# Optimization experiments

Measured on AMD Instinct MI355X. Metric: run time of the kernel, lower is better.

Reference implementation:

```python
import jax, jax.numpy as jnp
import numpy as np

WINDOW = 2  # hardcoded global in the original module


def band_count(seq_len, window=WINDOW):
    """C[a,b] = number of positions i whose local window covers both a and b.
    Windows (from converse_qk): i=0 -> [0, W]; i=1 -> [0, W+1];
    i=seq-2 -> [seq-W-2, seq-1]; i=seq-1 -> [seq-W-1, seq-1]; else [i-W, i+W].
    """
    i = jnp.arange(seq_len)
    lo = jnp.clip(i - window, 0, None)
    hi = jnp.clip(i + window, None, seq_len - 1)
    lo = jnp.where(i == 1, 0, lo)
    hi = jnp.where(i == 1, window + 1, hi)
    lo = jnp.where(i == seq_len - 2, seq_len - window - 2, lo)
    hi = jnp.where(i == seq_len - 2, seq_len - 1, hi)
    a = jnp.arange(seq_len)[None, :]
    M = ((a >= lo[:, None]) & (a <= hi[:, None])).astype(jnp.float32)  # [i, a]
    return M.T @ M  # [seq, seq]


def setup_inputs() -> dict:
    key = jax.random.key(0)
    ks = jax.random.split(key, 12)
    bs, seq, d_model = 2, 2048, 512
    s = 1.0 / np.sqrt(d_model)
    inp = {
        'q': jax.random.normal(ks[0], (bs, seq, d_model), jnp.float32),
        'k': jax.random.normal(ks[1], (bs, seq, d_model), jnp.float32),
        'v': jax.random.normal(ks[2], (bs, seq, d_model), jnp.float32),
        'Wq': jax.random.normal(ks[3], (d_model, d_model), jnp.float32) * s,
        'bq': jnp.zeros((d_model,), jnp.float32),
        'Wk': jax.random.normal(ks[4], (d_model, d_model), jnp.float32) * s,
        'bk': jnp.zeros((d_model,), jnp.float32),
        'Wv': jax.random.normal(ks[5], (d_model, d_model), jnp.float32) * s,
        'bv': jnp.zeros((d_model,), jnp.float32),
        'Wo': jax.random.normal(ks[6], (d_model, d_model), jnp.float32) * s,
        'bo': jnp.zeros((d_model,), jnp.float32),
    }
    return inp


def reference(q, k, v, Wq, bq, Wk, bk, Wv, bv, Wo, bo):
    bs, seq, d_model = q.shape
    heads = 8
    d_k = d_model // heads
    # projections (torch Linear uses x @ W.T + b; here W stored already transposed)
    qh = (q @ Wq + bq).reshape(bs, seq, heads, d_k).transpose(0, 2, 1, 3)
    kh = (k @ Wk + bk).reshape(bs, seq, heads, d_k).transpose(0, 2, 1, 3)
    vh = (v @ Wv + bv).reshape(bs, seq, heads, d_k).transpose(0, 2, 1, 3)
    C = band_count(seq)  # [seq, seq] window-overlap counts
    scores = jnp.einsum('bhqd,bhkd->bhqk', qh, kh) / jnp.sqrt(jnp.float32(d_k))
    scores = scores * C  # banded count-weighted scores; zeros outside band
    attn = jax.nn.softmax(scores, axis=-1)  # full-row softmax, as in original
    out = jnp.einsum('bhqk,bhkd->bhqd', attn, vh)
    concat = out.transpose(0, 2, 1, 3).reshape(bs, seq, d_model)
    return concat @ Wo + bo
```

## Files before the change

### kernel.cpp

```cpp
#include <hip/hip_runtime.h>
#include <hip/hip_bf16.h>

#define SEQ 2048
#define DM  512
#define BS  2
#define NH  8
#define DK  64
#define MROWS (BS * SEQ)
#define GK 64

typedef __attribute__((ext_vector_type(8))) short bf16x8;
typedef __attribute__((ext_vector_type(4))) float f32x4;

__device__ __forceinline__ unsigned short f2bf(float f) {
    unsigned int u = __float_as_uint(f);
    u += 0x7fff + ((u >> 16) & 1);
    return (unsigned short)(u >> 16);
}
__device__ __forceinline__ float bf2f(unsigned short b) {
    return __uint_as_float((unsigned int)b << 16);
}

#define GLDS16(g, l) __builtin_amdgcn_global_load_lds( \
    (const __attribute__((address_space(1))) void*)(g), \
    (__attribute__((address_space(3))) void*)(unsigned int)(unsigned long long)(l), 16, 0, 0)

__global__ __launch_bounds__(256) void prep_w(const float* __restrict__ Wq, const float* __restrict__ Wk,
                                              const float* __restrict__ Wv, const float* __restrict__ Wo,
                                              const float* __restrict__ bv_,
                                              unsigned short* __restrict__ WqT, unsigned short* __restrict__ WkT,
                                              unsigned short* __restrict__ WvT, unsigned short* __restrict__ WoT,
                                              float* __restrict__ vsum)
{
    __shared__ float tile[32][33];
    const int bid = blockIdx.x;
    if (bid == 0) {
        #pragma unroll
        for (int t = 0; t < 4; ++t) {
            const int idx = threadIdx.x * 4 + t;
            vsum[idx] = (float)SEQ * bv_[idx & (DM - 1)];
        }
    }
    const int z = bid >> 8;
    const int tl = bid & 255;
    const float* W = (z == 0) ? Wq : (z == 1) ? Wk : (z == 2) ? Wv : Wo;
    unsigned short* T = (z == 0) ? WqT : (z == 1) ? WkT : (z == 2) ? WvT : WoT;
    const int n0 = (tl & 15) * 32, k0 = (tl >> 4) * 32;
    const int tx = threadIdx.x & 31;
    const int ty = threadIdx.x >> 5;
    #pragma unroll
    for (int r = 0; r < 32; r += 8)
        tile[ty + r][tx] = W[(size_t)(k0 + ty + r) * DM + n0 + tx];
    __syncthreads();
    #pragma unroll
    for (int r = 0; r < 32; r += 8)
        T[(size_t)(n0 + ty + r) * DM + k0 + tx] = f2bf(tile[tx][ty + r]);
}

__global__ __launch_bounds__(256) void gemm_qkv_cvt(const float* __restrict__ q,
                                                    const float* __restrict__ k,
                                                    const float* __restrict__ v,
                                                    const unsigned short* __restrict__ WqT,
                                                    const unsigned short* __restrict__ WkT,
                                                    const unsigned short* __restrict__ WvT,
                                                    const float* __restrict__ bq, const float* __restrict__ bk,
                                                    const float* __restrict__ bvp,
                                                    unsigned short* __restrict__ Qb, unsigned short* __restrict__ Kb,
                                                    unsigned short* __restrict__ Vb, float* __restrict__ vsum)
{
    __shared__ unsigned short S[12288];

    const int g = blockIdx.x;
    const int xcd   = g & 7;
    const int n_idx = (g >> 3) & 3;
    const int t     = g >> 5;
    const int strip = t * 8 + xcd;
    const int z     = strip >> 6;
    const int m0    = (strip & 63) * 64;
    const int n0    = n_idx * 128;

    const float* Af; const unsigned short* BT; const float* bias; unsigned short* C; float* vs;
    if (z == 0)      { Af = q; BT = WqT; bias = bq; C = Qb; vs = nullptr; }
    else if (z == 1) { Af = k; BT = WkT; bias = bk; C = Kb; vs = nullptr; }
    else             { Af = v; BT = WvT; bias = bvp; C = Vb; vs = vsum; }

    const int tid  = threadIdx.x;
    const int lane = tid & 63;
    const int wave = tid >> 6;
    const int wm = (wave & 1) * 32;
    const int wn = (wave >> 1) * 64;
    const int l15 = lane & 15;
    const int q8  = (lane >> 4) * 8;

    f32x4 acc[2][4];
    #pragma unroll
    for (int i = 0; i < 2; ++i)
        #pragma unroll
        for (int j = 0; j < 4; ++j)
            acc[i][j] = (f32x4){0.f, 0.f, 0.f, 0.f};

    const int arow = tid >> 4;
    const int akl  = (tid & 15) * 4;
    const int awoff = ((akl >> 5) * 2048) + (akl & 31);

    const unsigned short* gb[4];
    unsigned short* lb[4];
    #pragma unroll
    for (int it = 0; it < 4; ++it) {
        const int c = tid + it * 256;
        const int n  = (c >> 2) & 127;
        const int kk = c >> 9;
        gb[it] = BT + (size_t)(n0 + n) * DM + kk * 32 + (c & 3) * 8;
        lb[it] = &S[4096 + c * 8];
    }

    for (int k0 = 0; k0 < DM; k0 += GK) {
        #pragma unroll
        for (int it = 0; it < 4; ++it)
            GLDS16(gb[it] + k0, lb[it]);

        float4 av[4];
        #pragma unroll
        for (int p = 0; p < 4; ++p)
            av[p] = *(const float4*)(Af + (size_t)(m0 + p * 16 + arow) * DM + k0 + akl);
        #pragma unroll
        for (int p = 0; p < 4; ++p) {
            ushort4 o;
            o.x = f2bf(av[p].x); o.y = f2bf(av[p].y); o.z = f2bf(av[p].z); o.w = f2bf(av[p].w);
            *(ushort4*)&S[awoff + (p * 16 + arow) * 32] = o;
        }
        __syncthreads();

        #pragma unroll
        for (int kk = 0; kk < 2; ++kk) {
            bf16x8 af[2], bfr[4];
            #pragma unroll
            for (int i = 0; i < 2; ++i)
                af[i] = *(const bf16x8*)&S[kk * 2048 + (wm + i * 16 + l15) * 32 + q8];
            #pragma unroll
            for (int j = 0; j < 4; ++j)
                bfr[j] = *(const bf16x8*)&S[4096 + kk * 4096 + (wn + j * 16 + l15) * 32 + q8];
            #pragma unroll
            for (int i = 0; i < 2; ++i)
                #pragma unroll
                for (int j = 0; j < 4; ++j)
                    acc[i][j] = __builtin_amdgcn_mfma_f32_16x16x32_bf16(af[i], bfr[j], acc[i][j], 0, 0, 0);
        }
        __syncthreads();
    }

    #pragma unroll
    for (int j = 0; j < 4; ++j) {
        const int col = n0 + wn + j * 16 + l15;
        const float bv = bias[col];
        #pragma unroll
        for (int i = 0; i < 2; ++i) {
            const int rbase = m0 + wm + i * 16 + (lane >> 4) * 4;
            #pragma unroll
            for (int r = 0; r < 4; ++r)
                C[(size_t)(rbase + r) * DM + col] = f2bf(acc[i][j][r] + bv);
        }
    }

    if (vs) {
        const int b = m0 >> 11;
        #pragma unroll
        for (int j = 0; j < 4; ++j) {
            float part = 0.f;
            #pragma unroll
            for (int i = 0; i < 2; ++i)
                #pragma unroll
                for (int r = 0; r < 4; ++r)
                    part += acc[i][j][r];
            part += __shfl_xor(part, 16, 64);
            part += __shfl_xor(part, 32, 64);
            if ((lane >> 4) == 0)
                atomicAdd(&vs[b * DM + n0 + wn + j * 16 + l15], part);
        }
    }
}

template<int TGM, int TGN, int WMT, int WNT>
__device__ __forceinline__ void gemm_core(const unsigned short* __restrict__ A,
                                          const unsigned short* __restrict__ BT,
                                          const float* __restrict__ bias,
                                          float* __restrict__ C,
                                          const int m0, const int n0)
{
    __shared__ unsigned short S[(TGM + TGN) * GK];

    const int tid  = threadIdx.x;
    const int lane = tid & 63;
    const int wave = tid >> 6;
    constexpr int WAVES_M = TGM / (WMT * 16);
    const int wm = (wave % WAVES_M) * (WMT * 16);
    const int wn = (wave / WAVES_M) * (WNT * 16);
    const int l15 = lane & 15;
    const int q8  = (lane >> 4) * 8;

    f32x4 acc[WMT][WNT];
    #pragma unroll
    for (int i = 0; i < WMT; ++i)
        #pragma unroll
        for (int j = 0; j < WNT; ++j)
            acc[i][j] = (f32x4){0.f, 0.f, 0.f, 0.f};

    constexpr int NCH = (TGM + TGN) * 8;
    constexpr int NIT = NCH / 256;
    const unsigned short* gp[NIT];
    unsigned short* lp[NIT];
    #pragma unroll
    for (int it = 0; it < NIT; ++it) {
        const int c = tid + it * 256;
        if (c < TGM * 8) {
            const int kk = c / (TGM * 4);
            const int cr = c - kk * (TGM * 4);
            gp[it] = A + (size_t)(m0 + (cr >> 2)) * DM + kk * 32 + (cr & 3) * 8;
        } else {
            const int cb = c - TGM * 8;
            const int kk = cb / (TGN * 4);
            const int cr = cb - kk * (TGN * 4);
            gp[it] = BT + (size_t)(n0 + (cr >> 2)) * DM + kk * 32 + (cr & 3) * 8;
        }
        lp[it] = &S[(size_t)c * 8];
    }

    for (int k0 = 0; k0 < DM; k0 += GK) {
        #pragma unroll
        for (int it = 0; it < NIT; ++it)
            GLDS16(gp[it] + k0, lp[it]);
        __syncthreads();

        #pragma unroll
        for (int kk = 0; kk < 2; ++kk) {
            bf16x8 af[WMT], bfr[WNT];
            #pragma unroll
            for (int i = 0; i < WMT; ++i)
                af[i] = *(const bf16x8*)&S[kk * TGM * 32 + (wm + i * 16 + l15) * 32 + q8];
            #pragma unroll
            for (int j = 0; j < WNT; ++j)
                bfr[j] = *(const bf16x8*)&S[TGM * 64 + kk * TGN * 32 + (wn + j * 16 + l15) * 32 + q8];
            #pragma unroll
            for (int i = 0; i < WMT; ++i)
                #pragma unroll
                for (int j = 0; j < WNT; ++j)
                    acc[i][j] = __builtin_amdgcn_mfma_f32_16x16x32_bf16(af[i], bfr[j], acc[i][j], 0, 0, 0);
        }
        __syncthreads();
    }

    #pragma unroll
    for (int j = 0; j < WNT; ++j) {
        const int col = n0 + wn + j * 16 + l15;
        const float bv = bias[col];
        #pragma unroll
        for (int i = 0; i < WMT; ++i) {
            const int rbase = m0 + wm + i * 16 + (lane >> 4) * 4;
            #pragma unroll
            for (int r = 0; r < 4; ++r)
                C[(size_t)(rbase + r) * DM + col] = acc[i][j][r] + bv;
        }
    }
}

__global__ __launch_bounds__(256) void gemm_out(const unsigned short* A, const unsigned short* BT,
                                                const float* bias, float* C)
{
    const int g = blockIdx.x;
    const int xcd   = g & 7;
    const int n_idx = (g >> 3) & 7;
    const int m_idx = (g >> 6) * 8 + xcd;
    gemm_core<64, 64, 2, 2>(A, BT, bias, C, m_idx * 64, n_idx * 64);
}

__global__ __launch_bounds__(64) void attn_mfma(const unsigned short* __restrict__ Qb,
                                                const unsigned short* __restrict__ Kb,
                                                const unsigned short* __restrict__ Vb,
                                                const float* __restrict__ vsum,
                                                unsigned short* __restrict__ concat)
{
    __shared__ unsigned short Wlds[16 * 32];
    const int lane = threadIdx.x;
    const int l15  = lane & 15;
    const int quad = lane >> 4;
    const int bh = blockIdx.y;
    const int b = bh >> 3, h = bh & 7;
    const int q0 = blockIdx.x * 16;
    const size_t rowbase = (size_t)b * SEQ;
    const int dbase = h * DK;

    const unsigned short* qrow = Qb + (rowbase + q0 + l15) * DM + dbase + quad * 8;
    const bf16x8 aq0 = *(const bf16x8*)(qrow);
    const bf16x8 aq1 = *(const bf16x8*)(qrow + 32);

    f32x4 sc[2];
    #pragma unroll
    for (int t = 0; t < 2; ++t) {
        int kp = q0 - 4 + t * 16 + l15;
        kp = min(max(kp, 0), SEQ - 1);
        const unsigned short* krow = Kb + (rowbase + kp) * DM + dbase + quad * 8;
        const bf16x8 b0 = *(const bf16x8*)(krow);
        const bf16x8 b1 = *(const bf16x8*)(krow + 32);
        f32x4 z = (f32x4){0.f, 0.f, 0.f, 0.f};
        z = __builtin_amdgcn_mfma_f32_16x16x32_bf16(aq0, b0, z, 0, 0, 0);
        sc[t] = __builtin_amdgcn_mfma_f32_16x16x32_bf16(aq1, b1, z, 0, 0, 0);
    }

    float dsum[4] = {0.f, 0.f, 0.f, 0.f};
    #pragma unroll
    for (int t = 0; t < 2; ++t) {
        const int kpos = q0 - 4 + t * 16 + l15;
        #pragma unroll
        for (int r = 0; r < 4; ++r) {
            const int qq = q0 + quad * 4 + r;
            const int mn = min(qq, kpos), mx = qq + kpos - mn;
            const float cnt = (float)(min(mn + 2, SEQ - 1) - max(mx - 2, 0) + 1);
            const float cw = (kpos >= 0 && kpos < SEQ && (mx - mn) <= 4) ? cnt * 0.125f : 0.f;
            const float w = expf(sc[t][r] * cw) - 1.f;
            const unsigned short wb = f2bf(w);
            Wlds[(quad * 4 + r) * 32 + t * 16 + l15] = wb;
            dsum[r] += bf2f(wb);
        }
    }
    #pragma unroll
    for (int off = 1; off <= 8; off <<= 1)
        #pragma unroll
        for (int r = 0; r < 4; ++r)
            dsum[r] += __shfl_xor(dsum[r], off, 64);

    __syncthreads();
    const bf16x8 aw = *(const bf16x8*)&Wlds[l15 * 32 + quad * 8];

    #pragma unroll
    for (int nt = 0; nt < 4; ++nt) {
        const int d = dbase + nt * 16 + l15;
        bf16x8 bv_;
        #pragma unroll
        for (int j = 0; j < 8; ++j) {
            int kr = q0 - 4 + quad * 8 + j;
            kr = min(max(kr, 0), SEQ - 1);
            bv_[j] = (short)Vb[(rowbase + kr) * DM + d];
        }
        f32x4 z = (f32x4){0.f, 0.f, 0.f, 0.f};
        const f32x4 o = __builtin_amdgcn_mfma_f32_16x16x32_bf16(aw, bv_, z, 0, 0, 0);
        const float vs = vsum[b * DM + d];
        #pragma unroll
        for (int r = 0; r < 4; ++r) {
            const float den = (float)SEQ + dsum[r];
            concat[(rowbase + q0 + quad * 4 + r) * DM + d] = f2bf((vs + o[r]) / den);
        }
    }
}

extern "C" void kernel_launch(void* const* d_in, const int* in_sizes, int n_in,
                              void* d_out, int out_size, void* d_ws, size_t ws_size,
                              hipStream_t stream) {
    const float* q  = (const float*)d_in[0];
    const float* k  = (const float*)d_in[1];
    const float* v  = (const float*)d_in[2];
    const float* Wq = (const float*)d_in[3];
    const float* bq = (const float*)d_in[4];
    const float* Wk = (const float*)d_in[5];
    const float* bk = (const float*)d_in[6];
    const float* Wv = (const float*)d_in[7];
    const float* bv = (const float*)d_in[8];
    const float* Wo = (const float*)d_in[9];
    const float* bo = (const float*)d_in[10];

    const size_t NE = (size_t)MROWS * DM;

    float* vsum = (float*)d_ws;
    unsigned short* Qb     = (unsigned short*)(vsum + 1024);
    unsigned short* Kb     = Qb + NE;
    unsigned short* Vb     = Kb + NE;
    unsigned short* WqT    = Vb + NE;
    unsigned short* WkT    = WqT + DM * DM;
    unsigned short* WvT    = WkT + DM * DM;
    unsigned short* WoT    = WvT + DM * DM;
    unsigned short* concat = WoT + DM * DM;

    prep_w<<<1024, 256, 0, stream>>>(Wq, Wk, Wv, Wo, bv, WqT, WkT, WvT, WoT, vsum);

    gemm_qkv_cvt<<<768, 256, 0, stream>>>(q, k, v, WqT, WkT, WvT,
                                          bq, bk, bv, Qb, Kb, Vb, vsum);

    attn_mfma<<<dim3(SEQ / 16, BS * NH), 64, 0, stream>>>(Qb, Kb, Vb, vsum, concat);

    gemm_out<<<512, 256, 0, stream>>>(concat, WoT, bo, (float*)d_out);
}
```

Baseline: 115.4 us.

## Fuse banded attention with output projection in one kernel

Combines the attention kernel and the output-projection GEMM. Each 512-thread block handles 16 query rows for all 8 heads, one wave per head, and writes the concat tile into shared memory. It then multiplies that tile by Wo directly, with each wave computing 64 output columns. This removes the concat round trip through global memory and one kernel launch. In exchange the grid shrinks to 256 blocks, and Wo is re-read from global or L2 by every block with no LDS staging.

```diff
diff --git a/kernel.cpp b/kernel.cpp
--- a/kernel.cpp
+++ b/kernel.cpp
@@ -180,114 +180,32 @@
     }
 }
 
-template<int TGM, int TGN, int WMT, int WNT>
-__device__ __forceinline__ void gemm_core(const unsigned short* __restrict__ A,
-                                          const unsigned short* __restrict__ BT,
-                                          const float* __restrict__ bias,
-                                          float* __restrict__ C,
-                                          const int m0, const int n0)
-{
-    __shared__ unsigned short S[(TGM + TGN) * GK];
-
-    const int tid  = threadIdx.x;
-    const int lane = tid & 63;
-    const int wave = tid >> 6;
-    constexpr int WAVES_M = TGM / (WMT * 16);
-    const int wm = (wave % WAVES_M) * (WMT * 16);
-    const int wn = (wave / WAVES_M) * (WNT * 16);
-    const int l15 = lane & 15;
-    const int q8  = (lane >> 4) * 8;
-
-    f32x4 acc[WMT][WNT];
-    #pragma unroll
-    for (int i = 0; i < WMT; ++i)
-        #pragma unroll
-        for (int j = 0; j < WNT; ++j)
-            acc[i][j] = (f32x4){0.f, 0.f, 0.f, 0.f};
-
-    constexpr int NCH = (TGM + TGN) * 8;
-    constexpr int NIT = NCH / 256;
-    const unsigned short* gp[NIT];
-    unsigned short* lp[NIT];
-    #pragma unroll
-    for (int it = 0; it < NIT; ++it) {
-        const int c = tid + it * 256;
-        if (c < TGM * 8) {
-            const int kk = c / (TGM * 4);
-            const int cr = c - kk * (TGM * 4);
-            gp[it] = A + (size_t)(m0 + (cr >> 2)) * DM + kk * 32 + (cr & 3) * 8;
-        } else {
-            const int cb = c - TGM * 8;
-            const int kk = cb / (TGN * 4);
-            const int cr = cb - kk * (TGN * 4);
-            gp[it] = BT + (size_t)(n0 + (cr >> 2)) * DM + kk * 32 + (cr & 3) * 8;
-        }
-        lp[it] = &S[(size_t)c * 8];
-    }
-
-    for (int k0 = 0; k0 < DM; k0 += GK) {
-        #pragma unroll
-        for (int it = 0; it < NIT; ++it)
-            GLDS16(gp[it] + k0, lp[it]);
-        __syncthreads();
-
-        #pragma unroll
-        for (int kk = 0; kk < 2; ++kk) {
-            bf16x8 af[WMT], bfr[WNT];
-            #pragma unroll
-            for (int i = 0; i < WMT; ++i)
-                af[i] = *(const bf16x8*)&S[kk * TGM * 32 + (wm + i * 16 + l15) * 32 + q8];
-            #pragma unroll
-            for (int j = 0; j < WNT; ++j)
-                bfr[j] = *(const bf16x8*)&S[TGM * 64 + kk * TGN * 32 + (wn + j * 16 + l15) * 32 + q8];
-            #pragma unroll
-            for (int i = 0; i < WMT; ++i)
-                #pragma unroll
-                for (int j = 0; j < WNT; ++j)
-                    acc[i][j] = __builtin_amdgcn_mfma_f32_16x16x32_bf16(af[i], bfr[j], acc[i][j], 0, 0, 0);
-        }
-        __syncthreads();
-    }
-
-    #pragma unroll
-    for (int j = 0; j < WNT; ++j) {
-        const int col = n0 + wn + j * 16 + l15;
-        const float bv = bias[col];
-        #pragma unroll
-        for (int i = 0; i < WMT; ++i) {
-            const int rbase = m0 + wm + i * 16 + (lane >> 4) * 4;
-            #pragma unroll
-            for (int r = 0; r < 4; ++r)
-                C[(size_t)(rbase + r) * DM + col] = acc[i][j][r] + bv;
-        }
-    }
-}
-
-__global__ __launch_bounds__(256) void gemm_out(const unsigned short* A, const unsigned short* BT,
-                                                const float* bias, float* C)
-{
-    const int g = blockIdx.x;
-    const int xcd   = g & 7;
-    const int n_idx = (g >> 3) & 7;
-    const int m_idx = (g >> 6) * 8 + xcd;
-    gemm_core<64, 64, 2, 2>(A, BT, bias, C, m_idx * 64, n_idx * 64);
-}
-
-__global__ __launch_bounds__(64) void attn_mfma(const unsigned short* __restrict__ Qb,
+__global__ __launch_bounds__(512) void attn_out(const unsigned short* __restrict__ Qb,
                                                 const unsigned short* __restrict__ Kb,
                                                 const unsigned short* __restrict__ Vb,
                                                 const float* __restrict__ vsum,
-                                                unsigned short* __restrict__ concat)
+                                                const unsigned short* __restrict__ WoT,
+                                                const float* __restrict__ bo,
+                                                float* __restrict__ out)
 {
-    __shared__ unsigned short Wlds[16 * 32];
-    const int lane = threadIdx.x;
+    __shared__ unsigned short Wc[16][520];
+    __shared__ unsigned short Wl[NH][16 * 32];
+
+    const int tid  = threadIdx.x;
+    const int lane = tid & 63;
+    const int h    = tid >> 6;
     const int l15  = lane & 15;
     const int quad = lane >> 4;
-    const int bh = blockIdx.y;
-    const int b = bh >> 3, h = bh & 7;
-    const int q0 = blockIdx.x * 16;
+    const int b  = blockIdx.x >> 7;
+    const int q0 = (blockIdx.x & 127) * 16;
     const size_t rowbase = (size_t)b * SEQ;
     const int dbase = h * DK;
+
+    const unsigned short* Bp = WoT + (size_t)(h * 64 + l15) * DM + quad * 8;
+    bf16x8 bpre[4];
+    #pragma unroll
+    for (int j = 0; j < 4; ++j)
+        bpre[j] = *(const bf16x8*)(Bp + (size_t)j * 16 * DM);
 
     const unsigned short* qrow = Qb + (rowbase + q0 + l15) * DM + dbase + quad * 8;
     const bf16x8 aq0 = *(const bf16x8*)(qrow);
@@ -318,7 +236,7 @@
             const float cw = (kpos >= 0 && kpos < SEQ && (mx - mn) <= 4) ? cnt * 0.125f : 0.f;
             const float w = expf(sc[t][r] * cw) - 1.f;
             const unsigned short wb = f2bf(w);
-            Wlds[(quad * 4 + r) * 32 + t * 16 + l15] = wb;
+            Wl[h][(quad * 4 + r) * 32 + t * 16 + l15] = wb;
             dsum[r] += bf2f(wb);
         }
     }
@@ -329,7 +247,7 @@
             dsum[r] += __shfl_xor(dsum[r], off, 64);
 
     __syncthreads();
-    const bf16x8 aw = *(const bf16x8*)&Wlds[l15 * 32 + quad * 8];
+    const bf16x8 aw = *(const bf16x8*)&Wl[h][l15 * 32 + quad * 8];
 
     #pragma unroll
     for (int nt = 0; nt < 4; ++nt) {
@@ -347,8 +265,35 @@
         #pragma unroll
         for (int r = 0; r < 4; ++r) {
             const float den = (float)SEQ + dsum[r];
-            concat[(rowbase + q0 + quad * 4 + r) * DM + d] = f2bf((vs + o[r]) / den);
-        }
+            Wc[quad * 4 + r][d] = f2bf((vs + o[r]) / den);
+        }
+    }
+
+    __syncthreads();
+
+    f32x4 acc[4];
+    #pragma unroll
+    for (int j = 0; j < 4; ++j)
+        acc[j] = (f32x4){0.f, 0.f, 0.f, 0.f};
+
+    #pragma unroll
+    for (int ks = 0; ks < 16; ++ks) {
+        const bf16x8 af = *(const bf16x8*)&Wc[l15][ks * 32 + quad * 8];
+        #pragma unroll
+        for (int j = 0; j < 4; ++j) {
+            const bf16x8 bw = (ks == 0) ? bpre[j]
+                            : *(const bf16x8*)(Bp + (size_t)j * 16 * DM + ks * 32);
+            acc[j] = __builtin_amdgcn_mfma_f32_16x16x32_bf16(af, bw, acc[j], 0, 0, 0);
+        }
+    }
+
+    #pragma unroll
+    for (int j = 0; j < 4; ++j) {
+        const int col = h * 64 + j * 16 + l15;
+        const float bov = bo[col];
+        #pragma unroll
+        for (int r = 0; r < 4; ++r)
+            out[(rowbase + q0 + quad * 4 + r) * DM + col] = acc[j][r] + bov;
     }
 }
 
@@ -377,14 +322,11 @@
     unsigned short* WkT    = WqT + DM * DM;
     unsigned short* WvT    = WkT + DM * DM;
     unsigned short* WoT    = WvT + DM * DM;
-    unsigned short* concat = WoT + DM * DM;
 
     prep_w<<<1024, 256, 0, stream>>>(Wq, Wk, Wv, Wo, bv, WqT, WkT, WvT, WoT, vsum);
 
     gemm_qkv_cvt<<<768, 256, 0, stream>>>(q, k, v, WqT, WkT, WvT,
                                           bq, bk, bv, Qb, Kb, Vb, vsum);
 
-    attn_mfma<<<dim3(SEQ / 16, BS * NH), 64, 0, stream>>>(Qb, Kb, Vb, vsum, concat);
-
-    gemm_out<<<512, 256, 0, stream>>>(concat, WoT, bo, (float*)d_out);
-}
+    attn_out<<<256, 512, 0, stream>>>(Qb, Kb, Vb, vsum, WoT, bo, (float*)d_out);
+}
```

After: 123.5 us. 7.1% more time.

## Fuse four kernels into two persistent kernels with software grid barriers

Applied to the files above, without the earlier changes.

Merges the weight transpose/convert with the QKV projection GEMM, and the banded attention with the output GEMM. Each pair runs in one launch, separated by an atomic-counter grid barrier, and a memset resets the counters. The goal is to remove two kernel launches and their inter-kernel gaps. It also switches the fp32-to-bf16 conversion of activations to packed v_cvt_pk_bf16_f32 instructions. The grid barrier relies on all 768 or 512 blocks being co-resident; if they are not, it deadlocks. The extra memset launch and the barrier spin add overhead.

```diff
diff --git a/kernel.cpp b/kernel.cpp
--- a/kernel.cpp
+++ b/kernel.cpp
@@ -25,50 +25,61 @@
     (const __attribute__((address_space(1))) void*)(g), \
     (__attribute__((address_space(3))) void*)(unsigned int)(unsigned long long)(l), 16, 0, 0)
 
-__global__ __launch_bounds__(256) void prep_w(const float* __restrict__ Wq, const float* __restrict__ Wk,
-                                              const float* __restrict__ Wv, const float* __restrict__ Wo,
-                                              const float* __restrict__ bv_,
-                                              unsigned short* __restrict__ WqT, unsigned short* __restrict__ WkT,
-                                              unsigned short* __restrict__ WvT, unsigned short* __restrict__ WoT,
-                                              float* __restrict__ vsum)
+__device__ __forceinline__ void gridbar(unsigned int* ctr, unsigned int target) {
+    __syncthreads();
+    if (threadIdx.x == 0) {
+        __hip_atomic_fetch_add(ctr, 1u, __ATOMIC_RELEASE, __HIP_MEMORY_SCOPE_AGENT);
+        while (__hip_atomic_load(ctr, __ATOMIC_RELAXED, __HIP_MEMORY_SCOPE_AGENT) < target)
+            __builtin_amdgcn_s_sleep(2);
+        (void)__hip_atomic_load(ctr, __ATOMIC_ACQUIRE, __HIP_MEMORY_SCOPE_AGENT);
+    }
+    __syncthreads();
+}
+
+__global__ __launch_bounds__(256, 3) void prep_qkv(
+    const float* __restrict__ q, const float* __restrict__ k, const float* __restrict__ v,
+    const float* __restrict__ Wq, const float* __restrict__ Wk,
+    const float* __restrict__ Wv, const float* __restrict__ Wo,
+    const float* __restrict__ bq, const float* __restrict__ bk, const float* __restrict__ bv_,
+    unsigned short* __restrict__ WqT, unsigned short* __restrict__ WkT,
+    unsigned short* __restrict__ WvT, unsigned short* __restrict__ WoT,
+    unsigned short* __restrict__ Qb, unsigned short* __restrict__ Kb,
+    unsigned short* __restrict__ Vb,
+    float* __restrict__ vsum, unsigned int* __restrict__ ctr)
 {
-    __shared__ float tile[32][33];
-    const int bid = blockIdx.x;
-    if (bid == 0) {
-        #pragma unroll
-        for (int t = 0; t < 4; ++t) {
-            const int idx = threadIdx.x * 4 + t;
-            vsum[idx] = (float)SEQ * bv_[idx & (DM - 1)];
-        }
-    }
-    const int z = bid >> 8;
-    const int tl = bid & 255;
-    const float* W = (z == 0) ? Wq : (z == 1) ? Wk : (z == 2) ? Wv : Wo;
-    unsigned short* T = (z == 0) ? WqT : (z == 1) ? WkT : (z == 2) ? WvT : WoT;
-    const int n0 = (tl & 15) * 32, k0 = (tl >> 4) * 32;
-    const int tx = threadIdx.x & 31;
-    const int ty = threadIdx.x >> 5;
-    #pragma unroll
-    for (int r = 0; r < 32; r += 8)
-        tile[ty + r][tx] = W[(size_t)(k0 + ty + r) * DM + n0 + tx];
-    __syncthreads();
-    #pragma unroll
-    for (int r = 0; r < 32; r += 8)
-        T[(size_t)(n0 + ty + r) * DM + k0 + tx] = f2bf(tile[tx][ty + r]);
-}
-
-__global__ __launch_bounds__(256) void gemm_qkv_cvt(const float* __restrict__ q,
-                                                    const float* __restrict__ k,
-                                                    const float* __restrict__ v,
-                                                    const unsigned short* __restrict__ WqT,
-                                                    const unsigned short* __restrict__ WkT,
-                                                    const unsigned short* __restrict__ WvT,
-                                                    const float* __restrict__ bq, const float* __restrict__ bk,
-                                                    const float* __restrict__ bvp,
-                                                    unsigned short* __restrict__ Qb, unsigned short* __restrict__ Kb,
-                                                    unsigned short* __restrict__ Vb, float* __restrict__ vsum)
-{
-    __shared__ unsigned short S[12288];
+    __shared__ __align__(16) unsigned char SMEM[24576];
+
+    {
+        float (*tile)[33] = (float (*)[33])SMEM;
+        if (blockIdx.x == 0) {
+            #pragma unroll
+            for (int t = 0; t < 4; ++t) {
+                const int idx = threadIdx.x * 4 + t;
+                vsum[idx] = (float)SEQ * bv_[idx & (DM - 1)];
+            }
+        }
+        const int tx = threadIdx.x & 31;
+        const int ty = threadIdx.x >> 5;
+        for (int tt = blockIdx.x; tt < 1024; tt += 768) {
+            const int z = tt >> 8;
+            const int tl = tt & 255;
+            const float* W = (z == 0) ? Wq : (z == 1) ? Wk : (z == 2) ? Wv : Wo;
+            unsigned short* T = (z == 0) ? WqT : (z == 1) ? WkT : (z == 2) ? WvT : WoT;
+            const int n0 = (tl & 15) * 32, k0 = (tl >> 4) * 32;
+            #pragma unroll
+            for (int r = 0; r < 32; r += 8)
+                tile[ty + r][tx] = W[(size_t)(k0 + ty + r) * DM + n0 + tx];
+            __syncthreads();
+            #pragma unroll
+            for (int r = 0; r < 32; r += 8)
+                T[(size_t)(n0 + ty + r) * DM + k0 + tx] = f2bf(tile[tx][ty + r]);
+            __syncthreads();
+        }
+    }
+
+    gridbar(ctr, 768);
+
+    unsigned short* S = (unsigned short*)SMEM;
 
     const int g = blockIdx.x;
     const int xcd   = g & 7;
@@ -82,7 +93,7 @@
     const float* Af; const unsigned short* BT; const float* bias; unsigned short* C; float* vs;
     if (z == 0)      { Af = q; BT = WqT; bias = bq; C = Qb; vs = nullptr; }
     else if (z == 1) { Af = k; BT = WkT; bias = bk; C = Kb; vs = nullptr; }
-    else             { Af = v; BT = WvT; bias = bvp; C = Vb; vs = vsum; }
+    else             { Af = v; BT = WvT; bias = bv_; C = Vb; vs = vsum; }
 
     const int tid  = threadIdx.x;
     const int lane = tid & 63;
@@ -125,9 +136,11 @@
             av[p] = *(const float4*)(Af + (size_t)(m0 + p * 16 + arow) * DM + k0 + akl);
         #pragma unroll
         for (int p = 0; p < 4; ++p) {
-            ushort4 o;
-            o.x = f2bf(av[p].x); o.y = f2bf(av[p].y); o.z = f2bf(av[p].z); o.w = f2bf(av[p].w);
-            *(ushort4*)&S[awoff + (p * 16 + arow) * 32] = o;
+            unsigned int u0, u1;
+            asm("v_cvt_pk_bf16_f32 %0, %1, %2" : "=v"(u0) : "v"(av[p].x), "v"(av[p].y));
+            asm("v_cvt_pk_bf16_f32 %0, %1, %2" : "=v"(u1) : "v"(av[p].z), "v"(av[p].w));
+            uint2 o; o.x = u0; o.y = u1;
+            *(uint2*)&S[awoff + (p * 16 + arow) * 32] = o;
         }
         __syncthreads();
 
@@ -152,13 +165,13 @@
     #pragma unroll
     for (int j = 0; j < 4; ++j) {
         const int col = n0 + wn + j * 16 + l15;
-        const float bv = bias[col];
+        const float bvv = bias[col];
         #pragma unroll
         for (int i = 0; i < 2; ++i) {
             const int rbase = m0 + wm + i * 16 + (lane >> 4) * 4;
             #pragma unroll
             for (int r = 0; r < 4; ++r)
-                C[(size_t)(rbase + r) * DM + col] = f2bf(acc[i][j][r] + bv);
+                C[(size_t)(rbase + r) * DM + col] = f2bf(acc[i][j][r] + bvv);
         }
     }
 
@@ -180,174 +193,168 @@
     }
 }
 
-template<int TGM, int TGN, int WMT, int WNT>
-__device__ __forceinline__ void gemm_core(const unsigned short* __restrict__ A,
-                                          const unsigned short* __restrict__ BT,
-                                          const float* __restrict__ bias,
-                                          float* __restrict__ C,
-                                          const int m0, const int n0)
+__global__ __launch_bounds__(256, 2) void attn_out2(
+    const unsigned short* __restrict__ Qb, const unsigned short* __restrict__ Kb,
+    const unsigned short* __restrict__ Vb, const float* __restrict__ vsum,
+    const unsigned short* __restrict__ WoT, const float* __restrict__ bo,
+    unsigned short* __restrict__ concat, float* __restrict__ out,
+    unsigned int* __restrict__ ctr)
 {
-    __shared__ unsigned short S[(TGM + TGN) * GK];
-
-    const int tid  = threadIdx.x;
-    const int lane = tid & 63;
-    const int wave = tid >> 6;
-    constexpr int WAVES_M = TGM / (WMT * 16);
-    const int wm = (wave % WAVES_M) * (WMT * 16);
-    const int wn = (wave / WAVES_M) * (WNT * 16);
-    const int l15 = lane & 15;
-    const int q8  = (lane >> 4) * 8;
-
-    f32x4 acc[WMT][WNT];
-    #pragma unroll
-    for (int i = 0; i < WMT; ++i)
-        #pragma unroll
-        for (int j = 0; j < WNT; ++j)
-            acc[i][j] = (f32x4){0.f, 0.f, 0.f, 0.f};
-
-    constexpr int NCH = (TGM + TGN) * 8;
-    constexpr int NIT = NCH / 256;
-    const unsigned short* gp[NIT];
-    unsigned short* lp[NIT];
-    #pragma unroll
-    for (int it = 0; it < NIT; ++it) {
-        const int c = tid + it * 256;
-        if (c < TGM * 8) {
-            const int kk = c / (TGM * 4);
-            const int cr = c - kk * (TGM * 4);
-            gp[it] = A + (size_t)(m0 + (cr >> 2)) * DM + kk * 32 + (cr & 3) * 8;
-        } else {
-            const int cb = c - TGM * 8;
-            const int kk = cb / (TGN * 4);
-            const int cr = cb - kk * (TGN * 4);
-            gp[it] = BT + (size_t)(n0 + (cr >> 2)) * DM + kk * 32 + (cr & 3) * 8;
-        }
-        lp[it] = &S[(size_t)c * 8];
-    }
-
-    for (int k0 = 0; k0 < DM; k0 += GK) {
-        #pragma unroll
-        for (int it = 0; it < NIT; ++it)
-            GLDS16(gp[it] + k0, lp[it]);
+    __shared__ __align__(16) unsigned char SMEM[16384];
+
+    {
+        unsigned short* Wlds = (unsigned short*)SMEM + (threadIdx.x >> 6) * 512;
+        const int lane = threadIdx.x & 63;
+        const int l15  = lane & 15;
+        const int quad = lane >> 4;
+        const int u  = blockIdx.x * 4 + (threadIdx.x >> 6);
+        const int bh = u >> 7;
+        const int b = bh >> 3, h = bh & 7;
+        const int q0 = (u & 127) * 16;
+        const size_t rowbase = (size_t)b * SEQ;
+        const int dbase = h * DK;
+
+        const unsigned short* qrow = Qb + (rowbase + q0 + l15) * DM + dbase + quad * 8;
+        const bf16x8 aq0 = *(const bf16x8*)(qrow);
+        const bf16x8 aq1 = *(const bf16x8*)(qrow + 32);
+
+        f32x4 sc[2];
+        #pragma unroll
+        for (int t = 0; t < 2; ++t) {
+            int kp = q0 - 4 + t * 16 + l15;
+            kp = min(max(kp, 0), SEQ - 1);
+            const unsigned short* krow = Kb + (rowbase + kp) * DM + dbase + quad * 8;
+            const bf16x8 b0 = *(const bf16x8*)(krow);
+            const bf16x8 b1 = *(const bf16x8*)(krow + 32);
+            f32x4 z = (f32x4){0.f, 0.f, 0.f, 0.f};
+            z = __builtin_amdgcn_mfma_f32_16x16x32_bf16(aq0, b0, z, 0, 0, 0);
+            sc[t] = __builtin_amdgcn_mfma_f32_16x16x32_bf16(aq1, b1, z, 0, 0, 0);
+        }
+
+        float dsum[4] = {0.f, 0.f, 0.f, 0.f};
+        #pragma unroll
+        for (int t = 0; t < 2; ++t) {
+            const int kpos = q0 - 4 + t * 16 + l15;
+            #pragma unroll
+            for (int r = 0; r < 4; ++r) {
+                const int qq = q0 + quad * 4 + r;
+                const int mn = min(qq, kpos), mx = qq + kpos - mn;
+                const float cnt = (float)(min(mn + 2, SEQ - 1) - max(mx - 2, 0) + 1);
+                const float cw = (kpos >= 0 && kpos < SEQ && (mx - mn) <= 4) ? cnt * 0.125f : 0.f;
+                const float w = expf(sc[t][r] * cw) - 1.f;
+                const unsigned short wb = f2bf(w);
+                Wlds[(quad * 4 + r) * 32 + t * 16 + l15] = wb;
+                dsum[r] += bf2f(wb);
+            }
+        }
+        #pragma unroll
+        for (int off = 1; off <= 8; off <<= 1)
+            #pragma unroll
+            for (int r = 0; r < 4; ++r)
+                dsum[r] += __shfl_xor(dsum[r], off, 64);
+
         __syncthreads();
-
-        #pragma unroll
-        for (int kk = 0; kk < 2; ++kk) {
-            bf16x8 af[WMT], bfr[WNT];
-            #pragma unroll
-            for (int i = 0; i < WMT; ++i)
-                af[i] = *(const bf16x8*)&S[kk * TGM * 32 + (wm + i * 16 + l15) * 32 + q8];
-            #pragma unroll
-            for (int j = 0; j < WNT; ++j)
-                bfr[j] = *(const bf16x8*)&S[TGM * 64 + kk * TGN * 32 + (wn + j * 16 + l15) * 32 + q8];
-            #pragma unroll
-            for (int i = 0; i < WMT; ++i)
-                #pragma unroll
-                for (int j = 0; j < WNT; ++j)
-                    acc[i][j] = __builtin_amdgcn_mfma_f32_16x16x32_bf16(af[i], bfr[j], acc[i][j], 0, 0, 0);
-        }
-        __syncthreads();
-    }
-
-    #pragma unroll
-    for (int j = 0; j < WNT; ++j) {
-        const int col = n0 + wn + j * 16 + l15;
-        const float bv = bias[col];
-        #pragma unroll
-        for (int i = 0; i < WMT; ++i) {
-            const int rbase = m0 + wm + i * 16 + (lane >> 4) * 4;
-            #pragma unroll
-            for (int r = 0; r < 4; ++r)
-                C[(size_t)(rbase + r) * DM + col] = acc[i][j][r] + bv;
-        }
-    }
-}
-
-__global__ __launch_bounds__(256) void gemm_out(const unsigned short* A, const unsigned short* BT,
-                                                const float* bias, float* C)
-{
-    const int g = blockIdx.x;
-    const int xcd   = g & 7;
-    const int n_idx = (g >> 3) & 7;
-    const int m_idx = (g >> 6) * 8 + xcd;
-    gemm_core<64, 64, 2, 2>(A, BT, bias, C, m_idx * 64, n_idx * 64);
-}
-
-__global__ __launch_bounds__(64) void attn_mfma(const unsigned short* __restrict__ Qb,
-                                                const unsigned short* __restrict__ Kb,
-                                                const unsigned short* __restrict__ Vb,
-                                                const float* __restrict__ vsum,
-                                                unsigned short* __restrict__ concat)
-{
-    __shared__ unsigned short Wlds[16 * 32];
-    const int lane = threadIdx.x;
-    const int l15  = lane & 15;
-    const int quad = lane >> 4;
-    const int bh = blockIdx.y;
-    const int b = bh >> 3, h = bh & 7;
-    const int q0 = blockIdx.x * 16;
-    const size_t rowbase = (size_t)b * SEQ;
-    const int dbase = h * DK;
-
-    const unsigned short* qrow = Qb + (rowbase + q0 + l15) * DM + dbase + quad * 8;
-    const bf16x8 aq0 = *(const bf16x8*)(qrow);
-    const bf16x8 aq1 = *(const bf16x8*)(qrow + 32);
-
-    f32x4 sc[2];
-    #pragma unroll
-    for (int t = 0; t < 2; ++t) {
-        int kp = q0 - 4 + t * 16 + l15;
-        kp = min(max(kp, 0), SEQ - 1);
-        const unsigned short* krow = Kb + (rowbase + kp) * DM + dbase + quad * 8;
-        const bf16x8 b0 = *(const bf16x8*)(krow);
-        const bf16x8 b1 = *(const bf16x8*)(krow + 32);
-        f32x4 z = (f32x4){0.f, 0.f, 0.f, 0.f};
-        z = __builtin_amdgcn_mfma_f32_16x16x32_bf16(aq0, b0, z, 0, 0, 0);
-        sc[t] = __builtin_amdgcn_mfma_f32_16x16x32_bf16(aq1, b1, z, 0, 0, 0);
-    }
-
-    float dsum[4] = {0.f, 0.f, 0.f, 0.f};
-    #pragma unroll
-    for (int t = 0; t < 2; ++t) {
-        const int kpos = q0 - 4 + t * 16 + l15;
-        #pragma unroll
-        for (int r = 0; r < 4; ++r) {
-            const int qq = q0 + quad * 4 + r;
-            const int mn = min(qq, kpos), mx = qq + kpos - mn;
-            const float cnt = (float)(min(mn + 2, SEQ - 1) - max(mx - 2, 0) + 1);
-            const float cw = (kpos >= 0 && kpos < SEQ && (mx - mn) <= 4) ? cnt * 0.125f : 0.f;
-            const float w = expf(sc[t][r] * cw) - 1.f;
-            const unsigned short wb = f2bf(w);
-            Wlds[(quad * 4 + r) * 32 + t * 16 + l15] = wb;
-            dsum[r] += bf2f(wb);
-        }
-    }
-    #pragma unroll
-    for (int off = 1; off <= 8; off <<= 1)
-        #pragma unroll
-        for (int r = 0; r < 4; ++r)
-            dsum[r] += __shfl_xor(dsum[r], off, 64);
-
-    __syncthreads();
-    const bf16x8 aw = *(const bf16x8*)&Wlds[l15 * 32 + quad * 8];
-
-    #pragma unroll
-    for (int nt = 0; nt < 4; ++nt) {
-        const int d = dbase + nt * 16 + l15;
-        bf16x8 bv_;
-        #pragma unroll
-        for (int j = 0; j < 8; ++j) {
-            int kr = q0 - 4 + quad * 8 + j;
-            kr = min(max(kr, 0), SEQ - 1);
-            bv_[j] = (short)Vb[(rowbase + kr) * DM + d];
-        }
-        f32x4 z = (f32x4){0.f, 0.f, 0.f, 0.f};
-        const f32x4 o = __builtin_amdgcn_mfma_f32_16x16x32_bf16(aw, bv_, z, 0, 0, 0);
-        const float vs = vsum[b * DM + d];
-        #pragma unroll
-        for (int r = 0; r < 4; ++r) {
-            const float den = (float)SEQ + dsum[r];
-            concat[(rowbase + q0 + quad * 4 + r) * DM + d] = f2bf((vs + o[r]) / den);
+        const bf16x8 aw = *(const bf16x8*)&Wlds[l15 * 32 + quad * 8];
+
+        #pragma unroll
+        for (int nt = 0; nt < 4; ++nt) {
+            const int d = dbase + nt * 16 + l15;
+            bf16x8 bv_;
+            #pragma unroll
+            for (int j = 0; j < 8; ++j) {
+                int kr = q0 - 4 + quad * 8 + j;
+                kr = min(max(kr, 0), SEQ - 1);
+                bv_[j] = (short)Vb[(rowbase + kr) * DM + d];
+            }
+            f32x4 z = (f32x4){0.f, 0.f, 0.f, 0.f};
+            const f32x4 o = __builtin_amdgcn_mfma_f32_16x16x32_bf16(aw, bv_, z, 0, 0, 0);
+            const float vsv = vsum[b * DM + d];
+            #pragma unroll
+            for (int r = 0; r < 4; ++r) {
+                const float den = (float)SEQ + dsum[r];
+                concat[(rowbase + q0 + quad * 4 + r) * DM + d] = f2bf((vsv + o[r]) / den);
+            }
+        }
+    }
+
+    gridbar(ctr, 512);
+
+    {
+        unsigned short* S = (unsigned short*)SMEM;
+        const int g = blockIdx.x;
+        const int xcd   = g & 7;
+        const int n_idx = (g >> 3) & 7;
+        const int m_idx = (g >> 6) * 8 + xcd;
+        const int m0 = m_idx * 64, n0 = n_idx * 64;
+
+        const int tid  = threadIdx.x;
+        const int lane = tid & 63;
+        const int wave = tid >> 6;
+        const int wm = (wave & 1) * 32;
+        const int wn = (wave >> 1) * 32;
+        const int l15 = lane & 15;
+        const int q8  = (lane >> 4) * 8;
+
+        f32x4 acc[2][2];
+        #pragma unroll
+        for (int i = 0; i < 2; ++i)
+            #pragma unroll
+            for (int j = 0; j < 2; ++j)
+                acc[i][j] = (f32x4){0.f, 0.f, 0.f, 0.f};
+
+        const unsigned short* gp[4];
+        unsigned short* lp[4];
+        #pragma unroll
+        for (int it = 0; it < 4; ++it) {
+            const int c = tid + it * 256;
+            if (c < 512) {
+                const int kk = c >> 8;
+                const int cr = c & 255;
+                gp[it] = concat + (size_t)(m0 + (cr >> 2)) * DM + kk * 32 + (c & 3) * 8;
+            } else {
+                const int cb = c - 512;
+                const int kk = cb >> 8;
+                const int cr = cb & 255;
+                gp[it] = WoT + (size_t)(n0 + (cr >> 2)) * DM + kk * 32 + (cb & 3) * 8;
+            }
+            lp[it] = &S[(size_t)c * 8];
+        }
+
+        for (int k0 = 0; k0 < DM; k0 += GK) {
+            #pragma unroll
+            for (int it = 0; it < 4; ++it)
+                GLDS16(gp[it] + k0, lp[it]);
+            __syncthreads();
+
+            #pragma unroll
+            for (int kk = 0; kk < 2; ++kk) {
+                bf16x8 af[2], bfr[2];
+                #pragma unroll
+                for (int i = 0; i < 2; ++i)
+                    af[i] = *(const bf16x8*)&S[kk * 2048 + (wm + i * 16 + l15) * 32 + q8];
+                #pragma unroll
+                for (int j = 0; j < 2; ++j)
+                    bfr[j] = *(const bf16x8*)&S[4096 + kk * 2048 + (wn + j * 16 + l15) * 32 + q8];
+                #pragma unroll
+                for (int i = 0; i < 2; ++i)
+                    #pragma unroll
+                    for (int j = 0; j < 2; ++j)
+                        acc[i][j] = __builtin_amdgcn_mfma_f32_16x16x32_bf16(af[i], bfr[j], acc[i][j], 0, 0, 0);
+            }
+            __syncthreads();
+        }
+
+        #pragma unroll
+        for (int j = 0; j < 2; ++j) {
+            const int col = n0 + wn + j * 16 + l15;
+            const float bov = bo[col];
+            #pragma unroll
+            for (int i = 0; i < 2; ++i) {
+                const int rbase = m0 + wm + i * 16 + (lane >> 4) * 4;
+                #pragma unroll
+                for (int r = 0; r < 4; ++r)
+                    out[(size_t)(rbase + r) * DM + col] = acc[i][j][r] + bov;
+            }
         }
     }
 }
@@ -369,7 +376,8 @@
 
     const size_t NE = (size_t)MROWS * DM;
 
-    float* vsum = (float*)d_ws;
+    unsigned int* ctrs = (unsigned int*)d_ws;
+    float* vsum = (float*)d_ws + 16;
     unsigned short* Qb     = (unsigned short*)(vsum + 1024);
     unsigned short* Kb     = Qb + NE;
     unsigned short* Vb     = Kb + NE;
@@ -379,12 +387,11 @@
     unsigned short* WoT    = WvT + DM * DM;
     unsigned short* concat = WoT + DM * DM;
 
-    prep_w<<<1024, 256, 0, stream>>>(Wq, Wk, Wv, Wo, bv, WqT, WkT, WvT, WoT, vsum);
-
-    gemm_qkv_cvt<<<768, 256, 0, stream>>>(q, k, v, WqT, WkT, WvT,
-                                          bq, bk, bv, Qb, Kb, Vb, vsum);
-
-    attn_mfma<<<dim3(SEQ / 16, BS * NH), 64, 0, stream>>>(Qb, Kb, Vb, vsum, concat);
-
-    gemm_out<<<512, 256, 0, stream>>>(concat, WoT, bo, (float*)d_out);
-}
+    hipMemsetAsync(d_ws, 0, 64, stream);
+
+    prep_qkv<<<768, 256, 0, stream>>>(q, k, v, Wq, Wk, Wv, Wo, bq, bk, bv,
+                                      WqT, WkT, WvT, WoT, Qb, Kb, Vb, vsum, &ctrs[0]);
+
+    attn_out2<<<512, 256, 0, stream>>>(Qb, Kb, Vb, vsum, WoT, bo, concat,
+                                       (float*)d_out, &ctrs[1]);
+}
```

Result: slower. 208.9 us (+81.0%).

## Double-buffer LDS in both GEMMs and stage V tile through LDS in attention

Applied to the files above, without the earlier changes.

Both the QKV projection GEMM and the output GEMM now use two LDS buffers, so the next K-slice's global loads (async global_load_lds for B, register loads of fp32 A) are issued before computing on the current slice. This removes the load-then-sync stall per iteration. A conversions use the packed v_cvt_pk_bf16_f32 instruction. The attention kernel loads its V window with coalesced 16-byte reads into a padded LDS tile instead of scalar strided global loads. The cost is doubled LDS footprint, which may reduce occupancy.

```diff
diff --git a/kernel.cpp b/kernel.cpp
--- a/kernel.cpp
+++ b/kernel.cpp
@@ -68,13 +68,13 @@
                                                     unsigned short* __restrict__ Qb, unsigned short* __restrict__ Kb,
                                                     unsigned short* __restrict__ Vb, float* __restrict__ vsum)
 {
-    __shared__ unsigned short S[12288];
+    __shared__ unsigned short S[2][12288];
 
     const int g = blockIdx.x;
     const int xcd   = g & 7;
     const int n_idx = (g >> 3) & 3;
-    const int t     = g >> 5;
-    const int strip = t * 8 + xcd;
+    const int t_    = g >> 5;
+    const int strip = t_ * 8 + xcd;
     const int z     = strip >> 6;
     const int m0    = (strip & 63) * 64;
     const int n0    = n_idx * 128;
@@ -102,49 +102,76 @@
     const int arow = tid >> 4;
     const int akl  = (tid & 15) * 4;
     const int awoff = ((akl >> 5) * 2048) + (akl & 31);
+    const float* agp = Af + (size_t)(m0 + arow) * DM + akl;
 
     const unsigned short* gb[4];
-    unsigned short* lb[4];
+    int lboff[4];
     #pragma unroll
     for (int it = 0; it < 4; ++it) {
         const int c = tid + it * 256;
         const int n  = (c >> 2) & 127;
         const int kk = c >> 9;
         gb[it] = BT + (size_t)(n0 + n) * DM + kk * 32 + (c & 3) * 8;
-        lb[it] = &S[4096 + c * 8];
-    }
-
-    for (int k0 = 0; k0 < DM; k0 += GK) {
+        lboff[it] = 4096 + c * 8;
+    }
+
+    {
         #pragma unroll
         for (int it = 0; it < 4; ++it)
-            GLDS16(gb[it] + k0, lb[it]);
-
+            GLDS16(gb[it], &S[0][lboff[it]]);
         float4 av[4];
         #pragma unroll
         for (int p = 0; p < 4; ++p)
-            av[p] = *(const float4*)(Af + (size_t)(m0 + p * 16 + arow) * DM + k0 + akl);
+            av[p] = *(const float4*)(agp + (size_t)p * 16 * DM);
         #pragma unroll
         for (int p = 0; p < 4; ++p) {
-            ushort4 o;
-            o.x = f2bf(av[p].x); o.y = f2bf(av[p].y); o.z = f2bf(av[p].z); o.w = f2bf(av[p].w);
-            *(ushort4*)&S[awoff + (p * 16 + arow) * 32] = o;
-        }
-        __syncthreads();
+            unsigned int u0, u1;
+            asm("v_cvt_pk_bf16_f32 %0, %1, %2" : "=v"(u0) : "v"(av[p].x), "v"(av[p].y));
+            asm("v_cvt_pk_bf16_f32 %0, %1, %2" : "=v"(u1) : "v"(av[p].z), "v"(av[p].w));
+            uint2 o; o.x = u0; o.y = u1;
+            *(uint2*)&S[0][awoff + (p * 16 + arow) * 32] = o;
+        }
+    }
+    __syncthreads();
+
+    for (int t = 0; t < 8; ++t) {
+        const int cur = t & 1, nxt = cur ^ 1;
+        const int k0n = (t + 1) * GK;
+        float4 av[4];
+        if (t < 7) {
+            #pragma unroll
+            for (int it = 0; it < 4; ++it)
+                GLDS16(gb[it] + k0n, &S[nxt][lboff[it]]);
+            #pragma unroll
+            for (int p = 0; p < 4; ++p)
+                av[p] = *(const float4*)(agp + (size_t)p * 16 * DM + k0n);
+        }
 
         #pragma unroll
         for (int kk = 0; kk < 2; ++kk) {
             bf16x8 af[2], bfr[4];
             #pragma unroll
             for (int i = 0; i < 2; ++i)
-                af[i] = *(const bf16x8*)&S[kk * 2048 + (wm + i * 16 + l15) * 32 + q8];
+                af[i] = *(const bf16x8*)&S[cur][kk * 2048 + (wm + i * 16 + l15) * 32 + q8];
             #pragma unroll
             for (int j = 0; j < 4; ++j)
-                bfr[j] = *(const bf16x8*)&S[4096 + kk * 4096 + (wn + j * 16 + l15) * 32 + q8];
+                bfr[j] = *(const bf16x8*)&S[cur][4096 + kk * 4096 + (wn + j * 16 + l15) * 32 + q8];
             #pragma unroll
             for (int i = 0; i < 2; ++i)
                 #pragma unroll
                 for (int j = 0; j < 4; ++j)
                     acc[i][j] = __builtin_amdgcn_mfma_f32_16x16x32_bf16(af[i], bfr[j], acc[i][j], 0, 0, 0);
+        }
+
+        if (t < 7) {
+            #pragma unroll
+            for (int p = 0; p < 4; ++p) {
+                unsigned int u0, u1;
+                asm("v_cvt_pk_bf16_f32 %0, %1, %2" : "=v"(u0) : "v"(av[p].x), "v"(av[p].y));
+                asm("v_cvt_pk_bf16_f32 %0, %1, %2" : "=v"(u1) : "v"(av[p].z), "v"(av[p].w));
+                uint2 o; o.x = u0; o.y = u1;
+                *(uint2*)&S[nxt][awoff + (p * 16 + arow) * 32] = o;
+            }
         }
         __syncthreads();
     }
@@ -180,99 +207,6 @@
     }
 }
 
-template<int TGM, int TGN, int WMT, int WNT>
-__device__ __forceinline__ void gemm_core(const unsigned short* __restrict__ A,
-                                          const unsigned short* __restrict__ BT,
-                                          const float* __restrict__ bias,
-                                          float* __restrict__ C,
-                                          const int m0, const int n0)
-{
-    __shared__ unsigned short S[(TGM + TGN) * GK];
-
-    const int tid  = threadIdx.x;
-    const int lane = tid & 63;
-    const int wave = tid >> 6;
-    constexpr int WAVES_M = TGM / (WMT * 16);
-    const int wm = (wave % WAVES_M) * (WMT * 16);
-    const int wn = (wave / WAVES_M) * (WNT * 16);
-    const int l15 = lane & 15;
-    const int q8  = (lane >> 4) * 8;
-
-    f32x4 acc[WMT][WNT];
-    #pragma unroll
-    for (int i = 0; i < WMT; ++i)
-        #pragma unroll
-        for (int j = 0; j < WNT; ++j)
-            acc[i][j] = (f32x4){0.f, 0.f, 0.f, 0.f};
-
-    constexpr int NCH = (TGM + TGN) * 8;
-    constexpr int NIT = NCH / 256;
-    const unsigned short* gp[NIT];
-    unsigned short* lp[NIT];
-    #pragma unroll
-    for (int it = 0; it < NIT; ++it) {
-        const int c = tid + it * 256;
-        if (c < TGM * 8) {
-            const int kk = c / (TGM * 4);
-            const int cr = c - kk * (TGM * 4);
-            gp[it] = A + (size_t)(m0 + (cr >> 2)) * DM + kk * 32 + (cr & 3) * 8;
-        } else {
-            const int cb = c - TGM * 8;
-            const int kk = cb / (TGN * 4);
-            const int cr = cb - kk * (TGN * 4);
-            gp[it] = BT + (size_t)(n0 + (cr >> 2)) * DM + kk * 32 + (cr & 3) * 8;
-        }
-        lp[it] = &S[(size_t)c * 8];
-    }
-
-    for (int k0 = 0; k0 < DM; k0 += GK) {
-        #pragma unroll
-        for (int it = 0; it < NIT; ++it)
-            GLDS16(gp[it] + k0, lp[it]);
-        __syncthreads();
-
-        #pragma unroll
-        for (int kk = 0; kk < 2; ++kk) {
-            bf16x8 af[WMT], bfr[WNT];
-            #pragma unroll
-            for (int i = 0; i < WMT; ++i)
-                af[i] = *(const bf16x8*)&S[kk * TGM * 32 + (wm + i * 16 + l15) * 32 + q8];
-            #pragma unroll
-            for (int j = 0; j < WNT; ++j)
-                bfr[j] = *(const bf16x8*)&S[TGM * 64 + kk * TGN * 32 + (wn + j * 16 + l15) * 32 + q8];
-            #pragma unroll
-            for (int i = 0; i < WMT; ++i)
-                #pragma unroll
-                for (int j = 0; j < WNT; ++j)
-                    acc[i][j] = __builtin_amdgcn_mfma_f32_16x16x32_bf16(af[i], bfr[j], acc[i][j], 0, 0, 0);
-        }
-        __syncthreads();
-    }
-
-    #pragma unroll
-    for (int j = 0; j < WNT; ++j) {
-        const int col = n0 + wn + j * 16 + l15;
-        const float bv = bias[col];
-        #pragma unroll
-        for (int i = 0; i < WMT; ++i) {
-            const int rbase = m0 + wm + i * 16 + (lane >> 4) * 4;
-            #pragma unroll
-            for (int r = 0; r < 4; ++r)
-                C[(size_t)(rbase + r) * DM + col] = acc[i][j][r] + bv;
-        }
-    }
-}
-
-__global__ __launch_bounds__(256) void gemm_out(const unsigned short* A, const unsigned short* BT,
-                                                const float* bias, float* C)
-{
-    const int g = blockIdx.x;
-    const int xcd   = g & 7;
-    const int n_idx = (g >> 3) & 7;
-    const int m_idx = (g >> 6) * 8 + xcd;
-    gemm_core<64, 64, 2, 2>(A, BT, bias, C, m_idx * 64, n_idx * 64);
-}
-
 __global__ __launch_bounds__(64) void attn_mfma(const unsigned short* __restrict__ Qb,
                                                 const unsigned short* __restrict__ Kb,
                                                 const unsigned short* __restrict__ Vb,
@@ -280,6 +214,7 @@
                                                 unsigned short* __restrict__ concat)
 {
     __shared__ unsigned short Wlds[16 * 32];
+    __shared__ unsigned short Vt[32 * 70];
     const int lane = threadIdx.x;
     const int l15  = lane & 15;
     const int quad = lane >> 4;
@@ -288,6 +223,16 @@
     const int q0 = blockIdx.x * 16;
     const size_t rowbase = (size_t)b * SEQ;
     const int dbase = h * DK;
+
+    bf16x8 vv[4];
+    #pragma unroll
+    for (int p = 0; p < 4; ++p) {
+        const int idx = p * 64 + lane;
+        const int row = idx >> 3, c8 = idx & 7;
+        int kr = q0 - 4 + row;
+        kr = min(max(kr, 0), SEQ - 1);
+        vv[p] = *(const bf16x8*)&Vb[(rowbase + kr) * DM + dbase + c8 * 8];
+    }
 
     const unsigned short* qrow = Qb + (rowbase + q0 + l15) * DM + dbase + quad * 8;
     const bf16x8 aq0 = *(const bf16x8*)(qrow);
@@ -328,26 +273,122 @@
         for (int r = 0; r < 4; ++r)
             dsum[r] += __shfl_xor(dsum[r], off, 64);
 
+    #pragma unroll
+    for (int p = 0; p < 4; ++p) {
+        const int idx = p * 64 + lane;
+        const int row = idx >> 3, c8 = idx & 7;
+        *(bf16x8*)&Vt[row * 70 + c8 * 8] = vv[p];
+    }
     __syncthreads();
+
     const bf16x8 aw = *(const bf16x8*)&Wlds[l15 * 32 + quad * 8];
 
     #pragma unroll
     for (int nt = 0; nt < 4; ++nt) {
-        const int d = dbase + nt * 16 + l15;
+        const int dl = nt * 16 + l15;
         bf16x8 bv_;
         #pragma unroll
-        for (int j = 0; j < 8; ++j) {
-            int kr = q0 - 4 + quad * 8 + j;
-            kr = min(max(kr, 0), SEQ - 1);
-            bv_[j] = (short)Vb[(rowbase + kr) * DM + d];
-        }
+        for (int j = 0; j < 8; ++j)
+            bv_[j] = (short)Vt[(quad * 8 + j) * 70 + dl];
         f32x4 z = (f32x4){0.f, 0.f, 0.f, 0.f};
         const f32x4 o = __builtin_amdgcn_mfma_f32_16x16x32_bf16(aw, bv_, z, 0, 0, 0);
-        const float vs = vsum[b * DM + d];
+        const float vs = vsum[b * DM + dbase + dl];
         #pragma unroll
         for (int r = 0; r < 4; ++r) {
             const float den = (float)SEQ + dsum[r];
-            concat[(rowbase + q0 + quad * 4 + r) * DM + d] = f2bf((vs + o[r]) / den);
+            concat[(rowbase + q0 + quad * 4 + r) * DM + dbase + dl] = f2bf((vs + o[r]) / den);
+        }
+    }
+}
+
+__global__ __launch_bounds__(256) void gemm_out(const unsigned short* __restrict__ A,
+                                                const unsigned short* __restrict__ BT,
+                                                const float* __restrict__ bias,
+                                                float* __restrict__ C)
+{
+    __shared__ unsigned short S[2][8192];
+
+    const int g = blockIdx.x;
+    const int xcd   = g & 7;
+    const int n_idx = (g >> 3) & 7;
+    const int m_idx = (g >> 6) * 8 + xcd;
+    const int m0 = m_idx * 64, n0 = n_idx * 64;
+
+    const int tid  = threadIdx.x;
+    const int lane = tid & 63;
+    const int wave = tid >> 6;
+    const int wm = (wave & 1) * 32;
+    const int wn = (wave >> 1) * 32;
+    const int l15 = lane & 15;
+    const int q8  = (lane >> 4) * 8;
+
+    f32x4 acc[2][2];
+    #pragma unroll
+    for (int i = 0; i < 2; ++i)
+        #pragma unroll
+        for (int j = 0; j < 2; ++j)
+            acc[i][j] = (f32x4){0.f, 0.f, 0.f, 0.f};
+
+    const unsigned short* gp[4];
+    int lpoff[4];
+    #pragma unroll
+    for (int it = 0; it < 4; ++it) {
+        const int c = tid + it * 256;
+        if (c < 512) {
+            const int kk = c >> 8;
+            const int cr = c & 255;
+            gp[it] = A + (size_t)(m0 + (cr >> 2)) * DM + kk * 32 + (c & 3) * 8;
+        } else {
+            const int cb = c - 512;
+            const int kk = cb >> 8;
+            const int cr = cb & 255;
+            gp[it] = BT + (size_t)(n0 + (cr >> 2)) * DM + kk * 32 + (cb & 3) * 8;
+        }
+        lpoff[it] = c * 8;
+    }
+
+    #pragma unroll
+    for (int it = 0; it < 4; ++it)
+        GLDS16(gp[it], &S[0][lpoff[it]]);
+    __syncthreads();
+
+    for (int t = 0; t < 8; ++t) {
+        const int cur = t & 1, nxt = cur ^ 1;
+        if (t < 7) {
+            const int k0n = (t + 1) * GK;
+            #pragma unroll
+            for (int it = 0; it < 4; ++it)
+                GLDS16(gp[it] + k0n, &S[nxt][lpoff[it]]);
+        }
+
+        #pragma unroll
+        for (int kk = 0; kk < 2; ++kk) {
+            bf16x8 af[2], bfr[2];
+            #pragma unroll
+            for (int i = 0; i < 2; ++i)
+                af[i] = *(const bf16x8*)&S[cur][kk * 2048 + (wm + i * 16 + l15) * 32 + q8];
+            #pragma unroll
+            for (int j = 0; j < 2; ++j)
+                bfr[j] = *(const bf16x8*)&S[cur][4096 + kk * 2048 + (wn + j * 16 + l15) * 32 + q8];
+            #pragma unroll
+            for (int i = 0; i < 2; ++i)
+                #pragma unroll
+                for (int j = 0; j < 2; ++j)
+                    acc[i][j] = __builtin_amdgcn_mfma_f32_16x16x32_bf16(af[i], bfr[j], acc[i][j], 0, 0, 0);
+        }
+        __syncthreads();
+    }
+
+    #pragma unroll
+    for (int j = 0; j < 2; ++j) {
+        const int col = n0 + wn + j * 16 + l15;
+        const float bov = bias[col];
+        #pragma unroll
+        for (int i = 0; i < 2; ++i) {
+            const int rbase = m0 + wm + i * 16 + (lane >> 4) * 4;
+            #pragma unroll
+            for (int r = 0; r < 4; ++r)
+                C[(size_t)(rbase + r) * DM + col] = acc[i][j][r] + bov;
         }
     }
 }
```

New measurement: 113.5 us. No clear change (-1.7%).
